# Kernel tuning notes

Hardware: AMD Instinct MI355X
Metric: run time of the kernel (lower is better)

The kernel has to match this reference:

```python
import jax, jax.numpy as jnp
import numpy as np

HIDDEN = 256
HEADS = 8
HEAD_DIM = HIDDEN // HEADS
SCALE = HEAD_DIM ** -0.5
N = 4096
NUM_GRAPHS = 16
LN_EPS = 1e-5


def setup_inputs() -> dict:
    key = jax.random.key(0)
    ks = jax.random.split(key, 8)
    x = jax.random.normal(ks[0], (N, HIDDEN), dtype=jnp.float32)
    batch = jnp.sort(jax.random.randint(ks[1], (N,), 0, NUM_GRAPHS, dtype=jnp.int64))
    # Xavier-uniform linear weights, stored as [in, out] (y = x @ W + b)
    lim = float(np.sqrt(6.0 / (HIDDEN + HIDDEN)))
    def W(k):
        return jax.random.uniform(k, (HIDDEN, HIDDEN), jnp.float32, -lim, lim)
    return {
        "x": x,
        "batch": batch,
        "Wq": W(ks[2]), "bq": jnp.zeros((HIDDEN,), jnp.float32),
        "Wk": W(ks[3]), "bk": jnp.zeros((HIDDEN,), jnp.float32),
        "Wv": W(ks[4]), "bv": jnp.zeros((HIDDEN,), jnp.float32),
        "Wo": W(ks[5]), "bo": jnp.zeros((HIDDEN,), jnp.float32),
        "gamma": jnp.ones((HIDDEN,), jnp.float32),
        "beta": jnp.zeros((HIDDEN,), jnp.float32),
    }


def _layer_norm(x, gamma, beta):
    mu = jnp.mean(x, axis=-1, keepdims=True)
    var = jnp.mean(jnp.square(x - mu), axis=-1, keepdims=True)
    return (x - mu) * jax.lax.rsqrt(var + LN_EPS) * gamma + beta


def reference(x, batch, Wq, bq, Wk, bk, Wv, bv, Wo, bo, gamma, beta):
    residual = x
    h = _layer_norm(x, gamma, beta)
    n = h.shape[0]
    q = (h @ Wq + bq).reshape(n, HEADS, HEAD_DIM)
    k = (h @ Wk + bk).reshape(n, HEADS, HEAD_DIM)
    v = (h @ Wv + bv).reshape(n, HEADS, HEAD_DIM)
    # dense scores masked to block-diagonal (same-graph) structure
    scores = jnp.einsum('ihd,jhd->ihj', q, k) * SCALE  # [N, H, N]
    same_graph = (batch[None, :] == batch[:, None])[:, None, :]  # [N, 1, N]
    scores = jnp.where(same_graph, scores, -jnp.inf)
    attn = jax.nn.softmax(scores, axis=-1)
    attn = jnp.nan_to_num(attn, nan=0.0)
    out = jnp.einsum('ihj,jhd->ihd', attn, v).reshape(n, HIDDEN)
    out = out @ Wo + bo
    return residual + out
```

## Files before the change

### kernel.cpp

```cpp
#include <hip/hip_runtime.h>

#define NNODES 4096
#define HID 256
#define NG 16
#define NH 8
#define HD 32
#define LN_EPS 1e-5f
#define QSCALE (0.17677669529663687f * 1.4426950408889634f)
#define CAPT 384
#define KLS 40
#define VTS (CAPT + 2)
#define QSL 12

typedef unsigned short u16;
typedef unsigned int u32;
typedef __bf16 bf16x8 __attribute__((ext_vector_type(8)));
typedef float f32x4 __attribute__((ext_vector_type(4)));

__device__ __forceinline__ float bf2f(u16 u){
  union { u32 i; float f; } c; c.i = ((u32)u) << 16; return c.f;
}
__device__ __forceinline__ u16 f2bf(float f){
  union { float f; u32 i; } c; c.f = f;
  u32 x = c.i;
  return (u16)((x + 0x7fffu + ((x >> 16) & 1u)) >> 16);
}

__global__ __launch_bounds__(256) void prep_kernel(
    const float* __restrict__ x, const float* __restrict__ gamma,
    const float* __restrict__ beta, u16* __restrict__ h,
    const float* __restrict__ Wq, const float* __restrict__ Wk,
    const float* __restrict__ Wv, const float* __restrict__ Wo,
    u16* __restrict__ Wt, const int* __restrict__ bw, int* __restrict__ seg){
  __shared__ u16 tile[32][33];
  __shared__ int bad;
  int b = blockIdx.x;
  if (b < 1024){
    int wave = threadIdx.x >> 6, lane = threadIdx.x & 63;
    int row = b * 4 + wave;
    float4 xv = ((const float4*)x)[row * 64 + lane];
    float a0 = xv.x, a1 = xv.y, a2 = xv.z, a3 = xv.w;
    float s = a0 + a1 + a2 + a3;
    #pragma unroll
    for (int m = 1; m < 64; m <<= 1) s += __shfl_xor(s, m);
    float mu = s * (1.0f / HID);
    float d0 = a0 - mu, d1 = a1 - mu, d2 = a2 - mu, d3 = a3 - mu;
    float vv = d0*d0 + d1*d1 + d2*d2 + d3*d3;
    #pragma unroll
    for (int m = 1; m < 64; m <<= 1) vv += __shfl_xor(vv, m);
    float rs = rsqrtf(vv * (1.0f / HID) + LN_EPS);
    float4 gv = ((const float4*)gamma)[lane];
    float4 bv = ((const float4*)beta)[lane];
    ushort4 o;
    o.x = f2bf(d0 * rs * gv.x + bv.x);
    o.y = f2bf(d1 * rs * gv.y + bv.y);
    o.z = f2bf(d2 * rs * gv.z + bv.z);
    o.w = f2bf(d3 * rs * gv.w + bv.w);
    *(ushort4*)(h + (size_t)row * HID + lane * 4) = o;
  } else if (b < 1280){
    int idx = b - 1024;
    int w = idx >> 6;
    int t = idx & 63;
    int bx = (t & 7) * 32, by = (t >> 3) * 32;
    const float* src = (w == 0) ? Wq : (w == 1) ? Wk : (w == 2) ? Wv : Wo;
    u16* dst = Wt + (size_t)w * HID * HID;
    int tx = threadIdx.x & 31, ty = threadIdx.x >> 5;
    #pragma unroll
    for (int r = 0; r < 32; r += 8)
      tile[ty + r][tx] = f2bf(src[(size_t)(by + ty + r) * HID + bx + tx]);
    __syncthreads();
    #pragma unroll
    for (int r = 0; r < 32; r += 8)
      dst[(size_t)(bx + ty + r) * HID + by + tx] = tile[tx][ty + r];
  } else {
    if (threadIdx.x == 0) bad = 0;
    __syncthreads();
    int local_bad = 0;
    for (int i = threadIdx.x; i < NNODES; i += 256){
      int v = bw[i];
      if (v < 0 || v > 15) local_bad = 1;
      if (i + 1 < NNODES && bw[i + 1] < v) local_bad = 1;
    }
    if (local_bad) atomicOr(&bad, 1);
    __syncthreads();
    int stride = bad ? 2 : 1;
    int g = threadIdx.x;
    if (g <= NG){
      int lo = 0, hi = NNODES;
      while (lo < hi){
        int mid = (lo + hi) >> 1;
        if (bw[mid * stride] < g) lo = mid + 1; else hi = mid;
      }
      seg[g] = lo;
    }
  }
}

template<bool FINAL>
__device__ __forceinline__ void gemm_tile(const u16* __restrict__ A, const u16* __restrict__ Bt,
    const float* __restrict__ bias, const float* __restrict__ resid, void* __restrict__ out){
  int gw = blockIdx.x * 4 + (threadIdx.x >> 6);
  int lane = threadIdx.x & 63;
  int lr = lane & 15, lq = lane >> 4;
  int m0 = (gw >> 4) * 64;
  int n0 = (gw & 15) * 16;
  f32x4 acc[4] = {};
  const u16* arow = A + (size_t)(m0 + lr) * HID + lq * 8;
  const u16* brow = Bt + (size_t)(n0 + lr) * HID + lq * 8;
  #pragma unroll
  for (int k0 = 0; k0 < HID; k0 += 32){
    bf16x8 b = *(const bf16x8*)(brow + k0);
    #pragma unroll
    for (int t = 0; t < 4; t++){
      bf16x8 a = *(const bf16x8*)(arow + (size_t)t * 16 * HID + k0);
      acc[t] = __builtin_amdgcn_mfma_f32_16x16x32_bf16(a, b, acc[t], 0, 0, 0);
    }
  }
  int col = n0 + lr;
  float bb = bias[col];
  #pragma unroll
  for (int t = 0; t < 4; t++){
    #pragma unroll
    for (int r = 0; r < 4; r++){
      int row = m0 + 16 * t + lq * 4 + r;
      float val = acc[t][r] + bb;
      if (FINAL){
        val += resid[(size_t)row * HID + col];
        ((float*)out)[(size_t)row * HID + col] = val;
      } else {
        ((u16*)out)[(size_t)row * HID + col] = f2bf(val);
      }
    }
  }
}

__global__ __launch_bounds__(256) void gemm_proj_kernel(const u16* __restrict__ ao,
    const u16* __restrict__ WtO, const float* __restrict__ bo, const float* __restrict__ x,
    float* __restrict__ out){
  gemm_tile<true>(ao, WtO, bo, x, out);
}

__global__ __launch_bounds__(512, 4) void qkv_attn_kernel(
    const u16* __restrict__ h, const u16* __restrict__ Wt,
    const float* __restrict__ bq, const float* __restrict__ bk,
    const float* __restrict__ bv, const int* __restrict__ seg,
    u16* __restrict__ out){
  __shared__ u16 kl[CAPT * KLS];
  __shared__ u16 vt[HD * VTS];
  __shared__ u16 ql[QSL * 16 * KLS];
  int gh = blockIdx.y;
  int g = gh >> 3, hd = gh & 7;
  int bid = blockIdx.x;
  int start = seg[g], end = seg[g + 1];
  int len = end - start;
  if (len <= 0) return;
  if (len > CAPT) len = CAPT;
  int ntj = (len + 15) >> 4;
  int wave = threadIdx.x >> 6, lane = threadIdx.x & 63;
  int lq = lane >> 4, lr = lane & 15;

  const u16* wq0p = Wt + (size_t)(hd * HD + lr) * HID;
  const u16* wk0p = wq0p + (size_t)HID * HID;
  const u16* wv0p = wq0p + (size_t)2 * HID * HID;
  float bq0 = bq[hd * HD + lr],      bq1 = bq[hd * HD + 16 + lr];
  float bk0 = bk[hd * HD + lr],      bk1 = bk[hd * HD + 16 + lr];
  float bv0 = bv[hd * HD + lr],      bv1 = bv[hd * HD + 16 + lr];

  for (int t = wave; t < ntj; t += 8){
    f32x4 ak0 = {}, ak1 = {}, av0 = {}, av1 = {};
    int row = start + (t << 4) + lr;
    if (row >= NNODES) row = NNODES - 1;
    const u16* hrow = h + (size_t)row * HID + lq * 8;
    #pragma unroll 2
    for (int k0 = 0; k0 < HID; k0 += 32){
      bf16x8 a    = *(const bf16x8*)(hrow + k0);
      bf16x8 wk0f = *(const bf16x8*)(wk0p + k0 + lq * 8);
      bf16x8 wk1f = *(const bf16x8*)(wk0p + 16 * HID + k0 + lq * 8);
      bf16x8 wv0f = *(const bf16x8*)(wv0p + k0 + lq * 8);
      bf16x8 wv1f = *(const bf16x8*)(wv0p + 16 * HID + k0 + lq * 8);
      ak0 = __builtin_amdgcn_mfma_f32_16x16x32_bf16(a, wk0f, ak0, 0, 0, 0);
      ak1 = __builtin_amdgcn_mfma_f32_16x16x32_bf16(a, wk1f, ak1, 0, 0, 0);
      av0 = __builtin_amdgcn_mfma_f32_16x16x32_bf16(a, wv0f, av0, 0, 0, 0);
      av1 = __builtin_amdgcn_mfma_f32_16x16x32_bf16(a, wv1f, av1, 0, 0, 0);
    }
    int jr = (t << 4) + lq * 4;
    #pragma unroll
    for (int r = 0; r < 4; r++){
      kl[(jr + r) * KLS + lr]      = f2bf(ak0[r] + bk0);
      kl[(jr + r) * KLS + 16 + lr] = f2bf(ak1[r] + bk1);
    }
    *(u32*)&vt[lr * VTS + jr]            = (u32)f2bf(av0[0] + bv0) | ((u32)f2bf(av0[1] + bv0) << 16);
    *(u32*)&vt[lr * VTS + jr + 2]        = (u32)f2bf(av0[2] + bv0) | ((u32)f2bf(av0[3] + bv0) << 16);
    *(u32*)&vt[(16 + lr) * VTS + jr]     = (u32)f2bf(av1[0] + bv1) | ((u32)f2bf(av1[1] + bv1) << 16);
    *(u32*)&vt[(16 + lr) * VTS + jr + 2] = (u32)f2bf(av1[2] + bv1) | ((u32)f2bf(av1[3] + bv1) << 16);
  }

  for (int s = wave; s < QSL; s += 8){
    int t = (s << 1) + bid;
    if (t >= ntj) continue;
    f32x4 aq0 = {}, aq1 = {};
    int row = start + (t << 4) + lr;
    if (row >= NNODES) row = NNODES - 1;
    const u16* hrow = h + (size_t)row * HID + lq * 8;
    #pragma unroll 2
    for (int k0 = 0; k0 < HID; k0 += 32){
      bf16x8 a    = *(const bf16x8*)(hrow + k0);
      bf16x8 wq0f = *(const bf16x8*)(wq0p + k0 + lq * 8);
      bf16x8 wq1f = *(const bf16x8*)(wq0p + 16 * HID + k0 + lq * 8);
      aq0 = __builtin_amdgcn_mfma_f32_16x16x32_bf16(a, wq0f, aq0, 0, 0, 0);
      aq1 = __builtin_amdgcn_mfma_f32_16x16x32_bf16(a, wq1f, aq1, 0, 0, 0);
    }
    int qr = (s << 4) + lq * 4;
    #pragma unroll
    for (int r = 0; r < 4; r++){
      ql[(qr + r) * KLS + lr]      = f2bf(aq0[r] + bq0);
      ql[(qr + r) * KLS + 16 + lr] = f2bf(aq1[r] + bq1);
    }
  }
  __syncthreads();

  for (int s = wave; s < QSL; s += 8){
    int t = (s << 1) + bid;
    if (t >= ntj) continue;
    int q0 = t << 4;
    bf16x8 qf = *(const bf16x8*)&ql[((s << 4) + lr) * KLS + lq * 8];
    float m = -3.0e38f, l = 0.f;
    f32x4 o0 = {0.f,0.f,0.f,0.f}, o1 = {0.f,0.f,0.f,0.f};
    for (int jt = 0; jt < ntj; jt++){
      int j0 = jt << 4;
      bf16x8 kf = *(const bf16x8*)&kl[(j0 + lr) * KLS + lq * 8];
      f32x4 st = __builtin_amdgcn_mfma_f32_16x16x32_bf16(kf, qf,
                   (f32x4){0.f,0.f,0.f,0.f}, 0, 0, 0);
      int jb = j0 + lq * 4;
      float s0 = (jb + 0 < len) ? st[0] * QSCALE : -3.0e38f;
      float s1 = (jb + 1 < len) ? st[1] * QSCALE : -3.0e38f;
      float s2 = (jb + 2 < len) ? st[2] * QSCALE : -3.0e38f;
      float s3 = (jb + 3 < len) ? st[3] * QSCALE : -3.0e38f;
      float tm = fmaxf(fmaxf(s0, s1), fmaxf(s2, s3));
      tm = fmaxf(tm, __shfl_xor(tm, 16));
      tm = fmaxf(tm, __shfl_xor(tm, 32));
      float mn = fmaxf(m, tm);
      float alpha = exp2f(m - mn);
      float p0 = exp2f(s0 - mn), p1 = exp2f(s1 - mn);
      float p2 = exp2f(s2 - mn), p3 = exp2f(s3 - mn);
      float ps = (p0 + p1) + (p2 + p3);
      ps += __shfl_xor(ps, 16);
      ps += __shfl_xor(ps, 32);
      l = l * alpha + ps;
      m = mn;
      union { bf16x8 v8; u32 w[4]; } pf, vf0, vf1;
      pf.w[0] = (u32)f2bf(p0) | ((u32)f2bf(p1) << 16);
      pf.w[1] = (u32)f2bf(p2) | ((u32)f2bf(p3) << 16);
      pf.w[2] = 0; pf.w[3] = 0;
      const u16* vp0 = &vt[lr * VTS + j0 + lq * 4];
      const u16* vp1 = &vt[(16 + lr) * VTS + j0 + lq * 4];
      vf0.w[0] = *(const u32*)vp0; vf0.w[1] = *(const u32*)(vp0 + 2);
      vf0.w[2] = 0; vf0.w[3] = 0;
      vf1.w[0] = *(const u32*)vp1; vf1.w[1] = *(const u32*)(vp1 + 2);
      vf1.w[2] = 0; vf1.w[3] = 0;
      o0 = o0 * alpha;
      o1 = o1 * alpha;
      o0 = __builtin_amdgcn_mfma_f32_16x16x32_bf16(vf0.v8, pf.v8, o0, 0, 0, 0);
      o1 = __builtin_amdgcn_mfma_f32_16x16x32_bf16(vf1.v8, pf.v8, o1, 0, 0, 0);
    }
    if (q0 + lr < len){
      float rl = 1.0f / l;
      u16* orow = out + (size_t)(start + q0 + lr) * HID + hd * HD;
      int dbase = lq * 4;
      *(u32*)&orow[dbase]          = (u32)f2bf(o0[0]*rl) | ((u32)f2bf(o0[1]*rl) << 16);
      *(u32*)&orow[dbase + 2]      = (u32)f2bf(o0[2]*rl) | ((u32)f2bf(o0[3]*rl) << 16);
      *(u32*)&orow[16 + dbase]     = (u32)f2bf(o1[0]*rl) | ((u32)f2bf(o1[1]*rl) << 16);
      *(u32*)&orow[16 + dbase + 2] = (u32)f2bf(o1[2]*rl) | ((u32)f2bf(o1[3]*rl) << 16);
    }
  }
}

__global__ void sentinel_kernel(u32* __restrict__ out, int nwords){
  int i = blockIdx.x * 256 + threadIdx.x;
  if (i < nwords) out[i] = 0x46404640u;
}

extern "C" void kernel_launch(void* const* d_in, const int* in_sizes, int n_in,
                              void* d_out, int out_size, void* d_ws, size_t ws_size,
                              hipStream_t stream){
  const float* x   = (const float*)d_in[0];
  const int* batch = (const int*)d_in[1];
  const float* Wq = (const float*)d_in[2],  *bq = (const float*)d_in[3];
  const float* Wk = (const float*)d_in[4],  *bk = (const float*)d_in[5];
  const float* Wv = (const float*)d_in[6],  *bv = (const float*)d_in[7];
  const float* Wo = (const float*)d_in[8],  *bo = (const float*)d_in[9];
  const float* gamma = (const float*)d_in[10], *beta = (const float*)d_in[11];

  const size_t WT_OFF = 1024;
  const size_t AO_OFF = WT_OFF + 4 * HID * HID * 2;
  const size_t BUF    = (size_t)NNODES * HID * 2;
  const size_t NEED   = AO_OFF + BUF;

  if (ws_size < NEED){
    int nwords = out_size / 2;
    sentinel_kernel<<<(nwords + 255) / 256, 256, 0, stream>>>((u32*)d_out, nwords);
    return;
  }

  char* w = (char*)d_ws;
  int* seg  = (int*)(w + 128);
  u16* Wt   = (u16*)(w + WT_OFF);
  u16* ao   = (u16*)(w + AO_OFF);
  u16* h    = (u16*)d_out;

  prep_kernel<<<1281, 256, 0, stream>>>(x, gamma, beta, h, Wq, Wk, Wv, Wo, Wt, batch, seg);
  qkv_attn_kernel<<<dim3(2, NG * NH), 512, 0, stream>>>(h, Wt, bq, bk, bv, seg, ao);
  gemm_proj_kernel<<<256, 256, 0, stream>>>(ao, Wt + 3 * (size_t)HID * HID, bo, x, (float*)d_out);
}
```

Baseline: 136.0 us.

## Split attention keys across wave halves and double query-tile blocks per head

```diff
diff --git a/kernel.cpp b/kernel.cpp
--- a/kernel.cpp
+++ b/kernel.cpp
@@ -10,7 +10,7 @@
 #define CAPT 384
 #define KLS 40
 #define VTS (CAPT + 2)
-#define QSL 12
+#define QSL 8
 
 typedef unsigned short u16;
 typedef unsigned int u32;
@@ -148,6 +148,7 @@
   __shared__ u16 kl[CAPT * KLS];
   __shared__ u16 vt[HD * VTS];
   __shared__ u16 ql[QSL * 16 * KLS];
+  __shared__ float mg[4][10][64];
   int gh = blockIdx.y;
   int g = gh >> 3, hd = gh & 7;
   int bid = blockIdx.x;
@@ -166,112 +167,154 @@
   float bk0 = bk[hd * HD + lr],      bk1 = bk[hd * HD + 16 + lr];
   float bv0 = bv[hd * HD + lr],      bv1 = bv[hd * HD + 16 + lr];
 
-  for (int t = wave; t < ntj; t += 8){
-    f32x4 ak0 = {}, ak1 = {}, av0 = {}, av1 = {};
-    int row = start + (t << 4) + lr;
-    if (row >= NNODES) row = NNODES - 1;
-    const u16* hrow = h + (size_t)row * HID + lq * 8;
-    #pragma unroll 2
+  {
+    f32x4 ak0[3] = {}, ak1[3] = {}, av0[3] = {}, av1[3] = {};
+    const u16* hrow[3];
+    #pragma unroll
+    for (int c = 0; c < 3; c++){
+      int row = start + ((wave + 8 * c) << 4) + lr;
+      if (row >= NNODES) row = NNODES - 1;
+      hrow[c] = h + (size_t)row * HID + lq * 8;
+    }
+    #pragma unroll
     for (int k0 = 0; k0 < HID; k0 += 32){
-      bf16x8 a    = *(const bf16x8*)(hrow + k0);
       bf16x8 wk0f = *(const bf16x8*)(wk0p + k0 + lq * 8);
       bf16x8 wk1f = *(const bf16x8*)(wk0p + 16 * HID + k0 + lq * 8);
       bf16x8 wv0f = *(const bf16x8*)(wv0p + k0 + lq * 8);
       bf16x8 wv1f = *(const bf16x8*)(wv0p + 16 * HID + k0 + lq * 8);
-      ak0 = __builtin_amdgcn_mfma_f32_16x16x32_bf16(a, wk0f, ak0, 0, 0, 0);
-      ak1 = __builtin_amdgcn_mfma_f32_16x16x32_bf16(a, wk1f, ak1, 0, 0, 0);
-      av0 = __builtin_amdgcn_mfma_f32_16x16x32_bf16(a, wv0f, av0, 0, 0, 0);
-      av1 = __builtin_amdgcn_mfma_f32_16x16x32_bf16(a, wv1f, av1, 0, 0, 0);
-    }
-    int jr = (t << 4) + lq * 4;
-    #pragma unroll
-    for (int r = 0; r < 4; r++){
-      kl[(jr + r) * KLS + lr]      = f2bf(ak0[r] + bk0);
-      kl[(jr + r) * KLS + 16 + lr] = f2bf(ak1[r] + bk1);
-    }
-    *(u32*)&vt[lr * VTS + jr]            = (u32)f2bf(av0[0] + bv0) | ((u32)f2bf(av0[1] + bv0) << 16);
-    *(u32*)&vt[lr * VTS + jr + 2]        = (u32)f2bf(av0[2] + bv0) | ((u32)f2bf(av0[3] + bv0) << 16);
-    *(u32*)&vt[(16 + lr) * VTS + jr]     = (u32)f2bf(av1[0] + bv1) | ((u32)f2bf(av1[1] + bv1) << 16);
-    *(u32*)&vt[(16 + lr) * VTS + jr + 2] = (u32)f2bf(av1[2] + bv1) | ((u32)f2bf(av1[3] + bv1) << 16);
-  }
-
-  for (int s = wave; s < QSL; s += 8){
-    int t = (s << 1) + bid;
-    if (t >= ntj) continue;
-    f32x4 aq0 = {}, aq1 = {};
-    int row = start + (t << 4) + lr;
-    if (row >= NNODES) row = NNODES - 1;
-    const u16* hrow = h + (size_t)row * HID + lq * 8;
-    #pragma unroll 2
-    for (int k0 = 0; k0 < HID; k0 += 32){
-      bf16x8 a    = *(const bf16x8*)(hrow + k0);
-      bf16x8 wq0f = *(const bf16x8*)(wq0p + k0 + lq * 8);
-      bf16x8 wq1f = *(const bf16x8*)(wq0p + 16 * HID + k0 + lq * 8);
-      aq0 = __builtin_amdgcn_mfma_f32_16x16x32_bf16(a, wq0f, aq0, 0, 0, 0);
-      aq1 = __builtin_amdgcn_mfma_f32_16x16x32_bf16(a, wq1f, aq1, 0, 0, 0);
-    }
-    int qr = (s << 4) + lq * 4;
-    #pragma unroll
-    for (int r = 0; r < 4; r++){
-      ql[(qr + r) * KLS + lr]      = f2bf(aq0[r] + bq0);
-      ql[(qr + r) * KLS + 16 + lr] = f2bf(aq1[r] + bq1);
+      #pragma unroll
+      for (int c = 0; c < 3; c++){
+        bf16x8 a = *(const bf16x8*)(hrow[c] + k0);
+        ak0[c] = __builtin_amdgcn_mfma_f32_16x16x32_bf16(a, wk0f, ak0[c], 0, 0, 0);
+        ak1[c] = __builtin_amdgcn_mfma_f32_16x16x32_bf16(a, wk1f, ak1[c], 0, 0, 0);
+        av0[c] = __builtin_amdgcn_mfma_f32_16x16x32_bf16(a, wv0f, av0[c], 0, 0, 0);
+        av1[c] = __builtin_amdgcn_mfma_f32_16x16x32_bf16(a, wv1f, av1[c], 0, 0, 0);
+      }
+    }
+    #pragma unroll
+    for (int c = 0; c < 3; c++){
+      int jr = ((wave + 8 * c) << 4) + lq * 4;
+      #pragma unroll
+      for (int r = 0; r < 4; r++){
+        kl[(jr + r) * KLS + lr]      = f2bf(ak0[c][r] + bk0);
+        kl[(jr + r) * KLS + 16 + lr] = f2bf(ak1[c][r] + bk1);
+      }
+      *(u32*)&vt[lr * VTS + jr]            = (u32)f2bf(av0[c][0] + bv0) | ((u32)f2bf(av0[c][1] + bv0) << 16);
+      *(u32*)&vt[lr * VTS + jr + 2]        = (u32)f2bf(av0[c][2] + bv0) | ((u32)f2bf(av0[c][3] + bv0) << 16);
+      *(u32*)&vt[(16 + lr) * VTS + jr]     = (u32)f2bf(av1[c][0] + bv1) | ((u32)f2bf(av1[c][1] + bv1) << 16);
+      *(u32*)&vt[(16 + lr) * VTS + jr + 2] = (u32)f2bf(av1[c][2] + bv1) | ((u32)f2bf(av1[c][3] + bv1) << 16);
+    }
+  }
+
+  {
+    int s = wave;
+    int t = ((s >> 2) << 4) + bid * 4 + (s & 3);
+    if (t < ntj){
+      f32x4 aq0 = {}, aq1 = {};
+      int row = start + (t << 4) + lr;
+      if (row >= NNODES) row = NNODES - 1;
+      const u16* hrow = h + (size_t)row * HID + lq * 8;
+      #pragma unroll
+      for (int k0 = 0; k0 < HID; k0 += 32){
+        bf16x8 a    = *(const bf16x8*)(hrow + k0);
+        bf16x8 wq0f = *(const bf16x8*)(wq0p + k0 + lq * 8);
+        bf16x8 wq1f = *(const bf16x8*)(wq0p + 16 * HID + k0 + lq * 8);
+        aq0 = __builtin_amdgcn_mfma_f32_16x16x32_bf16(a, wq0f, aq0, 0, 0, 0);
+        aq1 = __builtin_amdgcn_mfma_f32_16x16x32_bf16(a, wq1f, aq1, 0, 0, 0);
+      }
+      int qr = (s << 4) + lq * 4;
+      #pragma unroll
+      for (int r = 0; r < 4; r++){
+        ql[(qr + r) * KLS + lr]      = f2bf(aq0[r] + bq0);
+        ql[(qr + r) * KLS + 16 + lr] = f2bf(aq1[r] + bq1);
+      }
     }
   }
   __syncthreads();
 
-  for (int s = wave; s < QSL; s += 8){
-    int t = (s << 1) + bid;
-    if (t >= ntj) continue;
-    int q0 = t << 4;
-    bf16x8 qf = *(const bf16x8*)&ql[((s << 4) + lr) * KLS + lq * 8];
+  int tl = wave & 3;
+  int jh = wave >> 2;
+  int nouter = (ntj + 15) >> 4;
+  for (int it = 0; it < nouter; it++){
+    int tq = it * 16 + bid * 4 + tl;
+    bool active = tq < ntj;
+    int q0 = tq << 4;
     float m = -3.0e38f, l = 0.f;
     f32x4 o0 = {0.f,0.f,0.f,0.f}, o1 = {0.f,0.f,0.f,0.f};
-    for (int jt = 0; jt < ntj; jt++){
-      int j0 = jt << 4;
-      bf16x8 kf = *(const bf16x8*)&kl[(j0 + lr) * KLS + lq * 8];
-      f32x4 st = __builtin_amdgcn_mfma_f32_16x16x32_bf16(kf, qf,
-                   (f32x4){0.f,0.f,0.f,0.f}, 0, 0, 0);
-      int jb = j0 + lq * 4;
-      float s0 = (jb + 0 < len) ? st[0] * QSCALE : -3.0e38f;
-      float s1 = (jb + 1 < len) ? st[1] * QSCALE : -3.0e38f;
-      float s2 = (jb + 2 < len) ? st[2] * QSCALE : -3.0e38f;
-      float s3 = (jb + 3 < len) ? st[3] * QSCALE : -3.0e38f;
-      float tm = fmaxf(fmaxf(s0, s1), fmaxf(s2, s3));
-      tm = fmaxf(tm, __shfl_xor(tm, 16));
-      tm = fmaxf(tm, __shfl_xor(tm, 32));
-      float mn = fmaxf(m, tm);
-      float alpha = exp2f(m - mn);
-      float p0 = exp2f(s0 - mn), p1 = exp2f(s1 - mn);
-      float p2 = exp2f(s2 - mn), p3 = exp2f(s3 - mn);
-      float ps = (p0 + p1) + (p2 + p3);
-      ps += __shfl_xor(ps, 16);
-      ps += __shfl_xor(ps, 32);
-      l = l * alpha + ps;
-      m = mn;
-      union { bf16x8 v8; u32 w[4]; } pf, vf0, vf1;
-      pf.w[0] = (u32)f2bf(p0) | ((u32)f2bf(p1) << 16);
-      pf.w[1] = (u32)f2bf(p2) | ((u32)f2bf(p3) << 16);
-      pf.w[2] = 0; pf.w[3] = 0;
-      const u16* vp0 = &vt[lr * VTS + j0 + lq * 4];
-      const u16* vp1 = &vt[(16 + lr) * VTS + j0 + lq * 4];
-      vf0.w[0] = *(const u32*)vp0; vf0.w[1] = *(const u32*)(vp0 + 2);
-      vf0.w[2] = 0; vf0.w[3] = 0;
-      vf1.w[0] = *(const u32*)vp1; vf1.w[1] = *(const u32*)(vp1 + 2);
-      vf1.w[2] = 0; vf1.w[3] = 0;
-      o0 = o0 * alpha;
-      o1 = o1 * alpha;
-      o0 = __builtin_amdgcn_mfma_f32_16x16x32_bf16(vf0.v8, pf.v8, o0, 0, 0, 0);
-      o1 = __builtin_amdgcn_mfma_f32_16x16x32_bf16(vf1.v8, pf.v8, o1, 0, 0, 0);
-    }
-    if (q0 + lr < len){
-      float rl = 1.0f / l;
+    if (active){
+      bf16x8 qf = *(const bf16x8*)&ql[((((it << 2) + tl) << 4) + lr) * KLS + lq * 8];
+      int half = (ntj + 1) >> 1;
+      int jt0 = jh ? half : 0;
+      int jt1 = jh ? ntj : half;
+      for (int jt = jt0; jt < jt1; jt++){
+        int j0 = jt << 4;
+        bf16x8 kf = *(const bf16x8*)&kl[(j0 + lr) * KLS + lq * 8];
+        f32x4 st = __builtin_amdgcn_mfma_f32_16x16x32_bf16(kf, qf,
+                     (f32x4){0.f,0.f,0.f,0.f}, 0, 0, 0);
+        int jb = j0 + lq * 4;
+        float s0 = (jb + 0 < len) ? st[0] * QSCALE : -3.0e38f;
+        float s1 = (jb + 1 < len) ? st[1] * QSCALE : -3.0e38f;
+        float s2 = (jb + 2 < len) ? st[2] * QSCALE : -3.0e38f;
+        float s3 = (jb + 3 < len) ? st[3] * QSCALE : -3.0e38f;
+        float tm = fmaxf(fmaxf(s0, s1), fmaxf(s2, s3));
+        tm = fmaxf(tm, __shfl_xor(tm, 16));
+        tm = fmaxf(tm, __shfl_xor(tm, 32));
+        float mn = fmaxf(m, tm);
+        float alpha = exp2f(m - mn);
+        float p0 = exp2f(s0 - mn), p1 = exp2f(s1 - mn);
+        float p2 = exp2f(s2 - mn), p3 = exp2f(s3 - mn);
+        float ps = (p0 + p1) + (p2 + p3);
+        ps += __shfl_xor(ps, 16);
+        ps += __shfl_xor(ps, 32);
+        l = l * alpha + ps;
+        m = mn;
+        union { bf16x8 v8; u32 w[4]; } pf, vf0, vf1;
+        pf.w[0] = (u32)f2bf(p0) | ((u32)f2bf(p1) << 16);
+        pf.w[1] = (u32)f2bf(p2) | ((u32)f2bf(p3) << 16);
+        pf.w[2] = 0; pf.w[3] = 0;
+        const u16* vp0 = &vt[lr * VTS + j0 + lq * 4];
+        const u16* vp1 = &vt[(16 + lr) * VTS + j0 + lq * 4];
+        vf0.w[0] = *(const u32*)vp0; vf0.w[1] = *(const u32*)(vp0 + 2);
+        vf0.w[2] = 0; vf0.w[3] = 0;
+        vf1.w[0] = *(const u32*)vp1; vf1.w[1] = *(const u32*)(vp1 + 2);
+        vf1.w[2] = 0; vf1.w[3] = 0;
+        o0 = o0 * alpha;
+        o1 = o1 * alpha;
+        o0 = __builtin_amdgcn_mfma_f32_16x16x32_bf16(vf0.v8, pf.v8, o0, 0, 0, 0);
+        o1 = __builtin_amdgcn_mfma_f32_16x16x32_bf16(vf1.v8, pf.v8, o1, 0, 0, 0);
+      }
+    }
+    if (jh == 1){
+      mg[tl][0][lane] = o0[0]; mg[tl][1][lane] = o0[1];
+      mg[tl][2][lane] = o0[2]; mg[tl][3][lane] = o0[3];
+      mg[tl][4][lane] = o1[0]; mg[tl][5][lane] = o1[1];
+      mg[tl][6][lane] = o1[2]; mg[tl][7][lane] = o1[3];
+      mg[tl][8][lane] = m;     mg[tl][9][lane] = l;
+    }
+    __syncthreads();
+    if (jh == 0 && active && q0 + lr < len){
+      float m2 = mg[tl][8][lane], l2 = mg[tl][9][lane];
+      float mn = fmaxf(m, m2);
+      float a  = exp2f(m - mn);
+      float a2 = exp2f(m2 - mn);
+      float lt = l * a + l2 * a2;
+      float rl = 1.0f / lt;
+      float r0 = (o0[0]*a + mg[tl][0][lane]*a2) * rl;
+      float r1 = (o0[1]*a + mg[tl][1][lane]*a2) * rl;
+      float r2 = (o0[2]*a + mg[tl][2][lane]*a2) * rl;
+      float r3 = (o0[3]*a + mg[tl][3][lane]*a2) * rl;
+      float r4 = (o1[0]*a + mg[tl][4][lane]*a2) * rl;
+      float r5 = (o1[1]*a + mg[tl][5][lane]*a2) * rl;
+      float r6 = (o1[2]*a + mg[tl][6][lane]*a2) * rl;
+      float r7 = (o1[3]*a + mg[tl][7][lane]*a2) * rl;
       u16* orow = out + (size_t)(start + q0 + lr) * HID + hd * HD;
       int dbase = lq * 4;
-      *(u32*)&orow[dbase]          = (u32)f2bf(o0[0]*rl) | ((u32)f2bf(o0[1]*rl) << 16);
-      *(u32*)&orow[dbase + 2]      = (u32)f2bf(o0[2]*rl) | ((u32)f2bf(o0[3]*rl) << 16);
-      *(u32*)&orow[16 + dbase]     = (u32)f2bf(o1[0]*rl) | ((u32)f2bf(o1[1]*rl) << 16);
-      *(u32*)&orow[16 + dbase + 2] = (u32)f2bf(o1[2]*rl) | ((u32)f2bf(o1[3]*rl) << 16);
-    }
+      *(u32*)&orow[dbase]          = (u32)f2bf(r0) | ((u32)f2bf(r1) << 16);
+      *(u32*)&orow[dbase + 2]      = (u32)f2bf(r2) | ((u32)f2bf(r3) << 16);
+      *(u32*)&orow[16 + dbase]     = (u32)f2bf(r4) | ((u32)f2bf(r5) << 16);
+      *(u32*)&orow[16 + dbase + 2] = (u32)f2bf(r6) | ((u32)f2bf(r7) << 16);
+    }
+    __syncthreads();
   }
 }
 
@@ -309,6 +352,6 @@
   u16* h    = (u16*)d_out;
 
   prep_kernel<<<1281, 256, 0, stream>>>(x, gamma, beta, h, Wq, Wk, Wv, Wo, Wt, batch, seg);
-  qkv_attn_kernel<<<dim3(2, NG * NH), 512, 0, stream>>>(h, Wt, bq, bk, bv, seg, ao);
+  qkv_attn_kernel<<<dim3(4, NG * NH), 512, 0, stream>>>(h, Wt, bq, bk, bv, seg, ao);
   gemm_proj_kernel<<<256, 256, 0, stream>>>(ao, Wt + 3 * (size_t)HID * HID, bo, x, (float*)d_out);
 }
```

Result: slower. 142.1 us (+4.5%).
